# Kernel optimization log

Measured on AMD Instinct MI355X. Metric: run time of the kernel, lower is better.

The kernel has to match this reference:

```python
import jax, jax.numpy as jnp
import numpy as np

NUM_GRAPHS = 128

def setup_inputs() -> dict:
    key = jax.random.key(0)
    ks = jax.random.split(key, 12)
    N, E = 50000, 800000
    x = jax.random.normal(ks[0], (N, 54), dtype=jnp.float32)
    edge_index = jax.random.randint(ks[1], (2, E), 0, N, dtype=jnp.int64)
    batch = jnp.sort(jax.random.randint(ks[2], (N,), 0, NUM_GRAPHS, dtype=jnp.int64))
    def lin(k, fi, fo):
        return jax.random.normal(k, (fi, fo), dtype=jnp.float32) / np.sqrt(fi)
    return {
        "x": x, "edge_index": edge_index, "batch": batch,
        "W1l": lin(ks[3], 54, 128), "b1": jnp.zeros((128,), jnp.float32), "W1r": lin(ks[4], 54, 128),
        "W2l": lin(ks[5], 128, 256), "b2": jnp.zeros((256,), jnp.float32), "W2r": lin(ks[6], 128, 256),
        "W3l": lin(ks[7], 256, 256), "b3": jnp.zeros((256,), jnp.float32), "W3r": lin(ks[8], 256, 256),
    }

def _sage(h, src, dst, n, Wl, b, Wr):
    # sum-aggregate neighbor features x_j (j=src) into node i (i=dst), then
    # out = lin_l(agg) + lin_r(h)  (PyG SAGEConv, aggr='sum')
    agg = jax.ops.segment_sum(h[src], dst, num_segments=n)
    return jax.nn.relu(agg @ Wl + b + h @ Wr)

def reference(x, edge_index, batch, W1l, b1, W1r, W2l, b2, W2r, W3l, b3, W3r):
    n = x.shape[0]
    src, dst = edge_index[0], edge_index[1]
    h = _sage(x, src, dst, n, W1l, b1, W1r)
    h = _sage(h, src, dst, n, W2l, b2, W2r)
    h = _sage(h, src, dst, n, W3l, b3, W3r)
    # global mean pool per graph (gep = global_mean_pool)
    sums = jax.ops.segment_sum(h, batch, num_segments=NUM_GRAPHS)
    cnts = jax.ops.segment_sum(jnp.ones((n, 1), h.dtype), batch, num_segments=NUM_GRAPHS)
    return sums / jnp.maximum(cnts, 1.0)
```

## Files before the change

### kernel.cpp

```cpp
#include <hip/hip_runtime.h>


typedef unsigned short u16;
typedef __attribute__((ext_vector_type(8))) short bf16x8;
typedef __attribute__((ext_vector_type(4))) float f32x4;

__device__ __forceinline__ u16 f2b(float f) {
    union { float f; unsigned u; } v; v.f = f;
    unsigned u = v.u;
    return (u16)((u + 0x7FFF + ((u >> 16) & 1)) >> 16);
}
__device__ __forceinline__ float b2f(u16 h) {
    union { unsigned u; float f; } v; v.u = ((unsigned)h) << 16;
    return v.f;
}

__global__ void k_prep(const float* __restrict__ x,
                       const float* __restrict__ W1l, const float* __restrict__ W1r,
                       const float* __restrict__ W2l, const float* __restrict__ W2r,
                       const float* __restrict__ W3l, const float* __restrict__ W3r,
                       u16* __restrict__ xb,
                       u16* __restrict__ wt1l, u16* __restrict__ wt1r,
                       u16* __restrict__ wt2l, u16* __restrict__ wt2r,
                       u16* __restrict__ wt3l, u16* __restrict__ wt3r, int N) {
    long idx = (long)blockIdx.x * 256 + threadIdx.x;
    long s0 = (long)N * 54;
    if (idx < s0) { xb[idx] = f2b(x[idx]); return; }
    idx -= s0;
    if (idx < 2 * 128 * 64) {
        u16* o = (idx < 128 * 64) ? wt1l : wt1r;
        const float* w = (idx < 128 * 64) ? W1l : W1r;
        long loc = idx % (128 * 64);
        int d = (int)(loc >> 6), k = (int)(loc & 63);
        o[loc] = (k < 54) ? f2b(w[(long)k * 128 + d]) : 0;
        return;
    }
    idx -= 2 * 128 * 64;
    if (idx < 2 * 256 * 128) {
        u16* o = (idx < 256 * 128) ? wt2l : wt2r;
        const float* w = (idx < 256 * 128) ? W2l : W2r;
        long loc = idx % (256 * 128);
        int d = (int)(loc >> 7), k = (int)(loc & 127);
        o[loc] = f2b(w[(long)k * 256 + d]);
        return;
    }
    idx -= 2 * 256 * 128;
    if (idx < 2 * 256 * 256) {
        u16* o = (idx < 256 * 256) ? wt3l : wt3r;
        const float* w = (idx < 256 * 256) ? W3l : W3r;
        long loc = idx % (256 * 256);
        int d = (int)(loc >> 8), k = (int)(loc & 255);
        o[loc] = f2b(w[(long)k * 256 + d]);
    }
}

__global__ void k_count(const int* __restrict__ dst, int* __restrict__ cnt, int E) {
    int e = blockIdx.x * 256 + threadIdx.x;
    if (e < E) atomicAdd(&cnt[dst[e]], 1);
}

__global__ void k_bsum(const int* __restrict__ cnt, int* __restrict__ bsum, int N) {
    __shared__ int sm[256];
    int i = blockIdx.x * 256 + threadIdx.x;
    sm[threadIdx.x] = (i < N) ? cnt[i] : 0;
    __syncthreads();
    for (int off = 128; off > 0; off >>= 1) {
        if (threadIdx.x < off) sm[threadIdx.x] += sm[threadIdx.x + off];
        __syncthreads();
    }
    if (threadIdx.x == 0) bsum[blockIdx.x] = sm[0];
}

__global__ void k_bscan(const int* __restrict__ bsum, int* __restrict__ boff, int NB) {
    __shared__ int sm[256];
    int t = threadIdx.x;
    int v = (t < NB) ? bsum[t] : 0;
    sm[t] = v;
    __syncthreads();
    for (int off = 1; off < 256; off <<= 1) {
        int add = (t >= off) ? sm[t - off] : 0;
        __syncthreads();
        sm[t] += add;
        __syncthreads();
    }
    if (t < NB) boff[t] = sm[t] - v;
}

__global__ void k_scan(const int* __restrict__ cnt, const int* __restrict__ boff,
                       int* __restrict__ rowptr, int* __restrict__ wpos, int N, int E) {
    __shared__ int sm[256];
    int t = threadIdx.x;
    int i = blockIdx.x * 256 + t;
    int v = (i < N) ? cnt[i] : 0;
    sm[t] = v;
    __syncthreads();
    for (int off = 1; off < 256; off <<= 1) {
        int add = (t >= off) ? sm[t - off] : 0;
        __syncthreads();
        sm[t] += add;
        __syncthreads();
    }
    int ex = sm[t] - v + boff[blockIdx.x];
    if (i < N) { rowptr[i] = ex; wpos[i] = ex; }
    if (i == 0) rowptr[N] = E;
}

__global__ void k_fill(const int* __restrict__ src, const int* __restrict__ dst,
                       int* __restrict__ wpos, int* __restrict__ csr, int E) {
    int e = blockIdx.x * 256 + threadIdx.x;
    if (e < E) {
        int p = atomicAdd(&wpos[dst[e]], 1);
        csr[p] = src[e];
    }
}

template <int D, int VEC>
__global__ __launch_bounds__(256) void k_agg(const u16* __restrict__ h,
                                             const int* __restrict__ rowptr,
                                             const int* __restrict__ csr,
                                             u16* __restrict__ agg, int n) {
    int w = threadIdx.x >> 6;
    int lane = threadIdx.x & 63;
    int i = blockIdx.x * 4 + w;
    if (i >= n) return;
    int b0 = rowptr[i], b1 = rowptr[i + 1];
    if constexpr (VEC == 4) {
        float a0 = 0.f, a1 = 0.f, a2 = 0.f, a3 = 0.f;
        #pragma unroll 4
        for (int b = b0; b < b1; ++b) {
            int s = csr[b];
            ushort4 v = *reinterpret_cast<const ushort4*>(h + (size_t)s * D + lane * 4);
            a0 += b2f(v.x); a1 += b2f(v.y); a2 += b2f(v.z); a3 += b2f(v.w);
        }
        ushort4 o; o.x = f2b(a0); o.y = f2b(a1); o.z = f2b(a2); o.w = f2b(a3);
        *reinterpret_cast<ushort4*>(agg + (size_t)i * D + lane * 4) = o;
    } else if constexpr (VEC == 2) {
        float a0 = 0.f, a1 = 0.f;
        #pragma unroll 4
        for (int b = b0; b < b1; ++b) {
            int s = csr[b];
            ushort2 v = *reinterpret_cast<const ushort2*>(h + (size_t)s * D + lane * 2);
            a0 += b2f(v.x); a1 += b2f(v.y);
        }
        ushort2 o; o.x = f2b(a0); o.y = f2b(a1);
        *reinterpret_cast<ushort2*>(agg + (size_t)i * D + lane * 2) = o;
    } else {
        if (lane < D) {
            float a0 = 0.f;
            #pragma unroll 4
            for (int b = b0; b < b1; ++b) {
                int s = csr[b];
                a0 += b2f(h[(size_t)s * D + lane]);
            }
            agg[(size_t)i * D + lane] = f2b(a0);
        }
    }
}

template <int KA, int KW, int DOUT, bool A16>
__global__ __launch_bounds__(256) void k_mgemm(const u16* __restrict__ A1,
                                               const u16* __restrict__ A2,
                                               const u16* __restrict__ Wt1,
                                               const u16* __restrict__ Wt2,
                                               const float* __restrict__ bias,
                                               u16* __restrict__ C, int N) {
    constexpr int BM = 128, BKP = 40;
    __shared__ u16 As[BM * BKP];
    __shared__ u16 Bs[BM * BKP];

    const int tid = threadIdx.x;
    const int w = tid >> 6, l = tid & 63;
    const int wr = w >> 1, wc = w & 1;
    const int lo = l & 15, hi = l >> 4;
    const int m0 = blockIdx.x * BM;
    const int n0 = blockIdx.y * 128;

    f32x4 acc[4][4];
    #pragma unroll
    for (int i = 0; i < 4; ++i)
        #pragma unroll
        for (int j = 0; j < 4; ++j) acc[i][j] = {0.f, 0.f, 0.f, 0.f};

    constexpr int KT = KW / 32;

    #pragma unroll
    for (int s = 0; s < 2; ++s) {
        const u16* __restrict__ Ap = s ? A2 : A1;
        const u16* __restrict__ Wp = s ? Wt2 : Wt1;
        for (int kt = 0; kt < KT; ++kt) {
            const int k0 = kt * 32;
            #pragma unroll
            for (int it = 0; it < 2; ++it) {
                int v = it * 256 + tid;
                int r = v >> 2, c = v & 3;
                uint4 val = *reinterpret_cast<const uint4*>(Wp + (size_t)(n0 + r) * KW + k0 + c * 8);
                *reinterpret_cast<uint4*>(&Bs[r * BKP + c * 8]) = val;
            }
            if constexpr (A16) {
                #pragma unroll
                for (int it = 0; it < 2; ++it) {
                    int v = it * 256 + tid;
                    int r = v >> 2, c = v & 3;
                    int m = m0 + r;
                    uint4 val = {0u, 0u, 0u, 0u};
                    if (m < N) val = *reinterpret_cast<const uint4*>(Ap + (size_t)m * KA + k0 + c * 8);
                    *reinterpret_cast<uint4*>(&As[r * BKP + c * 8]) = val;
                }
            } else {
                #pragma unroll
                for (int it = 0; it < 8; ++it) {
                    int v = it * 256 + tid;
                    int r = v >> 4, c = v & 15;
                    int m = m0 + r;
                    int k = k0 + c * 2;
                    unsigned val = 0;
                    if (m < N && k < KA)
                        val = *reinterpret_cast<const unsigned*>(Ap + (size_t)m * KA + k);
                    *reinterpret_cast<unsigned*>(&As[r * BKP + c * 2]) = val;
                }
            }
            __syncthreads();
            bf16x8 af[4], bf[4];
            #pragma unroll
            for (int f = 0; f < 4; ++f) {
                af[f] = *reinterpret_cast<const bf16x8*>(&Bs[(wc * 64 + f * 16 + lo) * BKP + hi * 8]);
                bf[f] = *reinterpret_cast<const bf16x8*>(&As[(wr * 64 + f * 16 + lo) * BKP + hi * 8]);
            }
            #pragma unroll
            for (int fm = 0; fm < 4; ++fm)
                #pragma unroll
                for (int fn = 0; fn < 4; ++fn)
                    acc[fm][fn] = __builtin_amdgcn_mfma_f32_16x16x32_bf16(af[fn], bf[fm], acc[fm][fn], 0, 0, 0);
            __syncthreads();
        }
    }
    #pragma unroll
    for (int fm = 0; fm < 4; ++fm) {
        int node = m0 + wr * 64 + fm * 16 + lo;
        if (node < N) {
            #pragma unroll
            for (int fn = 0; fn < 4; ++fn) {
                int fb = n0 + wc * 64 + fn * 16 + hi * 4;
                float4 bv = *reinterpret_cast<const float4*>(bias + fb);
                ushort4 o;
                o.x = f2b(fmaxf(acc[fm][fn][0] + bv.x, 0.f));
                o.y = f2b(fmaxf(acc[fm][fn][1] + bv.y, 0.f));
                o.z = f2b(fmaxf(acc[fm][fn][2] + bv.z, 0.f));
                o.w = f2b(fmaxf(acc[fm][fn][3] + bv.w, 0.f));
                *reinterpret_cast<ushort4*>(C + (size_t)node * DOUT + fb) = o;
            }
        }
    }
}

template <int ROWS>
__global__ void k_pool(const u16* __restrict__ h3, const int* __restrict__ batch,
                       float* __restrict__ outsum, int* __restrict__ cnt, int N) {
    int r0 = blockIdx.x * ROWS;
    int r1 = min(r0 + ROWS, N);
    if (r0 >= N) return;
    int d = threadIdx.x;
    int cur = batch[r0];
    float s = 0.f;
    int c = 0;
    for (int i = r0; i < r1; ++i) {
        int g = batch[i];
        if (g != cur) {
            atomicAdd(&outsum[cur * 256 + d], s);
            if (d == 0) atomicAdd(&cnt[cur], c);
            s = 0.f; c = 0; cur = g;
        }
        s += b2f(h3[(size_t)i * 256 + d]);
        c++;
    }
    atomicAdd(&outsum[cur * 256 + d], s);
    if (d == 0) atomicAdd(&cnt[cur], c);
}

__global__ void k_div(float* __restrict__ out, const int* __restrict__ cnt, int total) {
    int idx = blockIdx.x * 256 + threadIdx.x;
    if (idx < total) {
        float c = fmaxf((float)cnt[idx >> 8], 1.0f);
        out[idx] = out[idx] / c;
    }
}

extern "C" void kernel_launch(void* const* d_in, const int* in_sizes, int n_in,
                              void* d_out, int out_size, void* d_ws, size_t ws_size,
                              hipStream_t stream) {
    const float* x   = (const float*)d_in[0];
    const int* ei    = (const int*)d_in[1];
    const int* batch = (const int*)d_in[2];
    const float* W1l = (const float*)d_in[3];
    const float* b1  = (const float*)d_in[4];
    const float* W1r = (const float*)d_in[5];
    const float* W2l = (const float*)d_in[6];
    const float* b2  = (const float*)d_in[7];
    const float* W2r = (const float*)d_in[8];
    const float* W3l = (const float*)d_in[9];
    const float* b3  = (const float*)d_in[10];
    const float* W3r = (const float*)d_in[11];

    const int N = in_sizes[0] / 54;
    const int E = in_sizes[1] / 2;
    const int* src = ei;
    const int* dst = ei + E;

    u16* xb   = (u16*)d_ws;
    u16* bufA = xb + (size_t)N * 54;
    u16* buf1 = bufA + (size_t)N * 256;
    u16* buf2 = buf1 + (size_t)N * 256;
    u16* wt1l = buf2 + (size_t)N * 256;
    u16* wt1r = wt1l + 128 * 64;
    u16* wt2l = wt1r + 128 * 64;
    u16* wt2r = wt2l + 256 * 128;
    u16* wt3l = wt2r + 256 * 128;
    u16* wt3r = wt3l + 256 * 256;
    int* ip = (int*)(wt3r + 256 * 256);
    int* cntdeg  = ip; ip += N;
    int* rowptr  = ip; ip += N + 1;
    int* wpos    = ip; ip += N + 1;
    int* bsum    = ip; ip += 256;
    int* boff    = ip; ip += 256;
    int* cntpool = ip; ip += 128;
    int* csr     = ip;

    hipMemsetAsync(cntdeg, 0, (size_t)N * sizeof(int), stream);
    hipMemsetAsync(d_out, 0, (size_t)out_size * sizeof(float), stream);
    hipMemsetAsync(cntpool, 0, 128 * sizeof(int), stream);

    const int NB = (N + 255) / 256;
    const int EB = (E + 255) / 256;

    {
        long total = (long)N * 54 + 2L * 128 * 64 + 2L * 256 * 128 + 2L * 256 * 256;
        int g = (int)((total + 255) / 256);
        k_prep<<<g, 256, 0, stream>>>(x, W1l, W1r, W2l, W2r, W3l, W3r,
                                      xb, wt1l, wt1r, wt2l, wt2r, wt3l, wt3r, N);
    }

    k_count<<<EB, 256, 0, stream>>>(dst, cntdeg, E);
    k_bsum<<<NB, 256, 0, stream>>>(cntdeg, bsum, N);
    k_bscan<<<1, 256, 0, stream>>>(bsum, boff, NB);
    k_scan<<<NB, 256, 0, stream>>>(cntdeg, boff, rowptr, wpos, N, E);
    k_fill<<<EB, 256, 0, stream>>>(src, dst, wpos, csr, E);

    const int AGB = (N + 3) / 4;
    const int GX = (N + 127) / 128;

    k_agg<54, 1><<<AGB, 256, 0, stream>>>(xb, rowptr, csr, bufA, N);
    {
        dim3 g(GX, 1);
        k_mgemm<54, 64, 128, false><<<g, 256, 0, stream>>>(bufA, xb, wt1l, wt1r, b1, buf1, N);
    }
    k_agg<128, 2><<<AGB, 256, 0, stream>>>(buf1, rowptr, csr, bufA, N);
    {
        dim3 g(GX, 2);
        k_mgemm<128, 128, 256, true><<<g, 256, 0, stream>>>(bufA, buf1, wt2l, wt2r, b2, buf2, N);
    }
    k_agg<256, 4><<<AGB, 256, 0, stream>>>(buf2, rowptr, csr, bufA, N);
    {
        dim3 g(GX, 2);
        k_mgemm<256, 256, 256, true><<<g, 256, 0, stream>>>(bufA, buf2, wt3l, wt3r, b3, buf1, N);
    }

    k_pool<32><<<(N + 31) / 32, 256, 0, stream>>>(buf1, batch, (float*)d_out, cntpool, N);
    k_div<<<(out_size + 255) / 256, 256, 0, stream>>>((float*)d_out, cntpool, out_size);
}
```

Before: 358.7 us.

## Split neighbor aggregation into feature-column chunks across blocks for cache locality

```diff
diff --git a/kernel.cpp b/kernel.cpp
--- a/kernel.cpp
+++ b/kernel.cpp
@@ -12,6 +12,14 @@
 }
 __device__ __forceinline__ float b2f(u16 h) {
     union { unsigned u; float f; } v; v.u = ((unsigned)h) << 16;
+    return v.f;
+}
+__device__ __forceinline__ float blo(unsigned u) {
+    union { unsigned u; float f; } v; v.u = u << 16;
+    return v.f;
+}
+__device__ __forceinline__ float bhi(unsigned u) {
+    union { unsigned u; float f; } v; v.u = u & 0xffff0000u;
     return v.f;
 }
 
@@ -114,45 +122,67 @@
     }
 }
 
-template <int D, int VEC>
-__global__ __launch_bounds__(256) void k_agg(const u16* __restrict__ h,
-                                             const int* __restrict__ rowptr,
-                                             const int* __restrict__ csr,
-                                             u16* __restrict__ agg, int n) {
+__global__ __launch_bounds__(256) void k_agg54(const u16* __restrict__ h,
+                                               const int* __restrict__ rowptr,
+                                               const int* __restrict__ csr,
+                                               u16* __restrict__ agg, int n) {
+    constexpr int D = 54;
     int w = threadIdx.x >> 6;
     int lane = threadIdx.x & 63;
     int i = blockIdx.x * 4 + w;
     if (i >= n) return;
     int b0 = rowptr[i], b1 = rowptr[i + 1];
-    if constexpr (VEC == 4) {
-        float a0 = 0.f, a1 = 0.f, a2 = 0.f, a3 = 0.f;
-        #pragma unroll 4
+    if (lane < D) {
+        float a0 = 0.f;
+        #pragma unroll 8
         for (int b = b0; b < b1; ++b) {
             int s = csr[b];
-            ushort4 v = *reinterpret_cast<const ushort4*>(h + (size_t)s * D + lane * 4);
-            a0 += b2f(v.x); a1 += b2f(v.y); a2 += b2f(v.z); a3 += b2f(v.w);
-        }
-        ushort4 o; o.x = f2b(a0); o.y = f2b(a1); o.z = f2b(a2); o.w = f2b(a3);
-        *reinterpret_cast<ushort4*>(agg + (size_t)i * D + lane * 4) = o;
-    } else if constexpr (VEC == 2) {
+            a0 += b2f(h[(size_t)s * D + lane]);
+        }
+        agg[(size_t)i * D + lane] = f2b(a0);
+    }
+}
+
+template <int D, int CF>
+__global__ __launch_bounds__(512) void k_aggc(const u16* __restrict__ h,
+                                              const int* __restrict__ rowptr,
+                                              const int* __restrict__ csr,
+                                              u16* __restrict__ agg, int n) {
+    static_assert(D == CF * 8, "8 chunks");
+    constexpr int LPE = CF / 2;
+    constexpr int SLOTS = 64 / LPE;
+    const int chunk = blockIdx.x & 7;
+    const int grp = blockIdx.x >> 3;
+    const int w = threadIdx.x >> 6, lane = threadIdx.x & 63;
+    const int slot = lane / LPE;
+    const int fl = lane % LPE;
+    const int col = chunk * CF + fl * 2;
+
+    for (int t = 0; t < 8; ++t) {
+        int node = grp * 64 + w * 8 + t;
+        if (node >= n) continue;
+        int b0 = rowptr[node], b1 = rowptr[node + 1];
         float a0 = 0.f, a1 = 0.f;
-        #pragma unroll 4
-        for (int b = b0; b < b1; ++b) {
-            int s = csr[b];
-            ushort2 v = *reinterpret_cast<const ushort2*>(h + (size_t)s * D + lane * 2);
-            a0 += b2f(v.x); a1 += b2f(v.y);
-        }
-        ushort2 o; o.x = f2b(a0); o.y = f2b(a1);
-        *reinterpret_cast<ushort2*>(agg + (size_t)i * D + lane * 2) = o;
-    } else {
-        if (lane < D) {
-            float a0 = 0.f;
-            #pragma unroll 4
-            for (int b = b0; b < b1; ++b) {
-                int s = csr[b];
-                a0 += b2f(h[(size_t)s * D + lane]);
-            }
-            agg[(size_t)i * D + lane] = f2b(a0);
+        int b = b0;
+        #pragma unroll 2
+        for (; b + SLOTS <= b1; b += SLOTS) {
+            int s = csr[b + slot];
+            unsigned v = *reinterpret_cast<const unsigned*>(h + (size_t)s * D + col);
+            a0 += blo(v); a1 += bhi(v);
+        }
+        if (slot < b1 - b) {
+            int s = csr[b + slot];
+            unsigned v = *reinterpret_cast<const unsigned*>(h + (size_t)s * D + col);
+            a0 += blo(v); a1 += bhi(v);
+        }
+        #pragma unroll
+        for (int off = LPE; off < 64; off <<= 1) {
+            a0 += __shfl_xor(a0, off, 64);
+            a1 += __shfl_xor(a1, off, 64);
+        }
+        if (slot == 0) {
+            unsigned o = ((unsigned)f2b(a0)) | (((unsigned)f2b(a1)) << 16);
+            *reinterpret_cast<unsigned*>(agg + (size_t)node * D + col) = o;
         }
     }
 }
@@ -347,18 +377,19 @@
 
     const int AGB = (N + 3) / 4;
     const int GX = (N + 127) / 128;
-
-    k_agg<54, 1><<<AGB, 256, 0, stream>>>(xb, rowptr, csr, bufA, N);
+    const int CGB = 8 * ((N + 63) / 64);
+
+    k_agg54<<<AGB, 256, 0, stream>>>(xb, rowptr, csr, bufA, N);
     {
         dim3 g(GX, 1);
         k_mgemm<54, 64, 128, false><<<g, 256, 0, stream>>>(bufA, xb, wt1l, wt1r, b1, buf1, N);
     }
-    k_agg<128, 2><<<AGB, 256, 0, stream>>>(buf1, rowptr, csr, bufA, N);
+    k_aggc<128, 16><<<CGB, 512, 0, stream>>>(buf1, rowptr, csr, bufA, N);
     {
         dim3 g(GX, 2);
         k_mgemm<128, 128, 256, true><<<g, 256, 0, stream>>>(bufA, buf1, wt2l, wt2r, b2, buf2, N);
     }
-    k_agg<256, 4><<<AGB, 256, 0, stream>>>(buf2, rowptr, csr, bufA, N);
+    k_aggc<256, 32><<<CGB, 512, 0, stream>>>(buf2, rowptr, csr, bufA, N);
     {
         dim3 g(GX, 2);
         k_mgemm<256, 256, 256, true><<<g, 256, 0, stream>>>(bufA, buf2, wt3l, wt3r, b3, buf1, N);
```

Measured after the change: 496.4 us. 1.38x slower.
